# Performance work log

Hardware: AMD Instinct MI355X
Metric: run time of the kernel (lower is better)

Reference implementation:

```python
import jax, jax.numpy as jnp
import numpy as np

# Constants from the module's docstrings / vm_step / constants
VOCAB = 272
D_MODEL = 512
CODE_START = 256  # Token.CODE_START (first special after 256 byte tokens)
CODE_END = 257    # Token.CODE_END
MEM = 258         # Token.MEM
ADDR_KEY = 206    # _SetDim.ADDR_KEY (48 dims: 3 nibbles x 16 one-hot)
MEM_STORE = 455   # _SetDim.MEM_STORE
BYTES_PER_INSTR = 5
INSTR_WIDTH = 8


def setup_inputs() -> dict:
    key = jax.random.key(0)
    k1, k2 = jax.random.split(key)
    token_ids = jax.random.randint(k1, (32, 8192), 0, VOCAB)
    embed_table = jax.random.normal(k2, (VOCAB, D_MODEL), dtype=jnp.float32)
    return {"token_ids": token_ids, "embed_table": embed_table, "mem_history_end": 2048}


def reference(token_ids, embed_table, mem_history_end):
    B, S = token_ids.shape
    x = embed_table[token_ids]                     # [B, S, D] gather
    pos = jnp.arange(S)

    # ---- ADDR_KEY injection (vectorized replacement of the per-token loop) ----
    is_cs = token_ids == CODE_START
    is_ce = token_ids == CODE_END
    # most recent CODE_START position at or before i (-1 if none yet)
    cs = jax.lax.cummax(jnp.where(is_cs, pos[None, :], -1), axis=1)       # [B, S]
    # the python loop breaks the row at the FIRST CODE_END
    first_ce = jnp.min(jnp.where(is_ce, pos[None, :], S), axis=1, keepdims=True)  # [B, 1]
    is_byte = token_ids < 256
    mask = (cs >= 0) & (pos[None, :] < first_ce) & is_byte                # [B, S]

    seq_pos = jnp.maximum(pos[None, :] - cs - 1, 0)                       # >=0 where mask
    addr = (seq_pos // BYTES_PER_INSTR) * INSTR_WIDTH + seq_pos % BYTES_PER_INSTR
    lo = addr & 15
    hi = (addr >> 4) & 15
    top = (addr >> 8) & 15

    nib = jnp.arange(16)
    onehot48 = jnp.concatenate(
        [lo[..., None] == nib, hi[..., None] == nib, top[..., None] == nib], axis=-1
    )  # [B, S, 48] bool

    seg = x[..., ADDR_KEY:ADDR_KEY + 48]
    seg = jnp.where(mask[..., None] & onehot48, jnp.float32(1.0), seg)
    x = x.at[..., ADDR_KEY:ADDR_KEY + 48].set(seg)

    # ---- MEM_STORE injection on historical MEM markers ----
    mem_mask = (token_ids == MEM) & (pos[None, :] < mem_history_end)
    ch = jnp.where(mem_mask, jnp.float32(1.0), x[..., MEM_STORE])
    x = x.at[..., MEM_STORE].set(ch)
    return x
```

## Files before the change

### kernel.cpp

```cpp
#include <hip/hip_runtime.h>
#include <hip/hip_bf16.h>

#define B 32
#define S 8192
#define D 512
#define CODE_START 256
#define CODE_END 257
#define MEM_TOK 258
#define ADDR_KEY 206
#define MEM_STORE 455
#define CHUNK 512
#define NCH (S / CHUNK)

typedef float f32x4 __attribute__((ext_vector_type(4)));

__global__ __launch_bounds__(256) void nvm_chunk_scan(
    const int* __restrict__ tok, int* __restrict__ cs_local,
    int* __restrict__ carry, int* __restrict__ mince) {
  const int c = blockIdx.x;
  const int b = blockIdx.y;
  const int tid = threadIdx.x;
  const int lane = tid & 63;
  const int wid = tid >> 6;
  const int base = c * CHUNK;
  const int* row = tok + b * S;

  const int s0 = base + 2 * tid, s1 = s0 + 1;
  const int t0 = row[s0], t1 = row[s1];
  int v0 = (t0 == CODE_START) ? s0 : -1;
  int v1 = (t1 == CODE_START) ? s1 : -1;
  const int i1 = max(v0, v1);

  int incl = i1;
  #pragma unroll
  for (int off = 1; off < 64; off <<= 1) {
    int u = __shfl_up(incl, off, 64);
    if (lane >= off) incl = max(incl, u);
  }
  int ex = __shfl_up(incl, 1, 64);
  if (lane == 0) ex = -1;

  int m = min((t0 == CODE_END) ? s0 : S, (t1 == CODE_END) ? s1 : S);
  #pragma unroll
  for (int off = 32; off; off >>= 1) m = min(m, __shfl_down(m, off, 64));

  __shared__ int wt[4], wm[4];
  if (lane == 63) wt[wid] = incl;
  if (lane == 0) wm[wid] = m;
  __syncthreads();

  int pre = -1;
  for (int w = 0; w < wid; ++w) pre = max(pre, wt[w]);
  ex = max(ex, pre);
  cs_local[b * S + s0] = max(ex, v0);
  cs_local[b * S + s1] = max(ex, i1);

  if (tid == 0) {
    carry[b * NCH + c] = max(max(wt[0], wt[1]), max(wt[2], wt[3]));
    mince[b * NCH + c] = min(min(wm[0], wm[1]), min(wm[2], wm[3]));
  }
}

__global__ __launch_bounds__(256) void nvm_main(
    const int* __restrict__ tok, const float* __restrict__ table,
    const int* __restrict__ cs_local, const int* __restrict__ carry,
    const int* __restrict__ mince, const int* __restrict__ mhe_p,
    float* __restrict__ out) {
  __shared__ int pre_sh[B * NCH];
  __shared__ int fce_sh[B];

  for (int i = threadIdx.x; i < B * NCH; i += 256) {
    const int b = i >> 4, c = i & (NCH - 1);
    int run = -1;
    for (int c2 = 0; c2 < c; ++c2) run = max(run, carry[(b << 4) + c2]);
    pre_sh[i] = run;
  }
  if (threadIdx.x < B) {
    int mn = S;
    #pragma unroll
    for (int c2 = 0; c2 < NCH; ++c2) mn = min(mn, mince[(threadIdx.x << 4) + c2]);
    fce_sh[threadIdx.x] = mn;
  }
  __syncthreads();

  const int lane = threadIdx.x & 127;
  const int half = threadIdx.x >> 7;
  const int mhe = mhe_p[0];
  const int NTP = B * S / 2;
  const int c0 = lane * 4;

  for (int tp = blockIdx.x; tp < NTP; tp += gridDim.x) {
    const int t = tp * 2 + half;
    const int b = t >> 13;
    const int s = t & (S - 1);

    const int tk = tok[t];
    const int cs = max(cs_local[t], pre_sh[(b << 4) + (s >> 9)]);
    const int f = fce_sh[b];

    const bool maskAddr = (cs >= 0) && (s < f) && (tk < 256);
    int c1 = -1, c2 = -1, c3 = -1;
    if (maskAddr) {
      int sp = s - cs - 1;
      if (sp < 0) sp = 0;
      int q = sp / 5;
      int r = sp - q * 5;
      int addr = q * 8 + r;
      c1 = ADDR_KEY + (addr & 15);
      c2 = ADDR_KEY + 16 + ((addr >> 4) & 15);
      c3 = ADDR_KEY + 32 + ((addr >> 8) & 15);
    }
    const bool memM = (tk == MEM_TOK) && (s < mhe);

    f32x4 v = *reinterpret_cast<const f32x4*>(table + tk * D + c0);
    #pragma unroll
    for (int j = 0; j < 4; ++j) {
      int ch = c0 + j;
      bool hit = (maskAddr && (ch == c1 || ch == c2 || ch == c3)) ||
                 (memM && ch == MEM_STORE);
      if (hit) v[j] = 1.0f;
    }
    f32x4* dst = reinterpret_cast<f32x4*>(out + (size_t)t * D + c0);
    __builtin_nontemporal_store(v, dst);
  }
}

extern "C" void kernel_launch(void* const* d_in, const int* in_sizes, int n_in,
                              void* d_out, int out_size, void* d_ws, size_t ws_size,
                              hipStream_t stream) {
  const int* tok = (const int*)d_in[0];
  const float* table = (const float*)d_in[1];
  const int* mhe = (const int*)d_in[2];
  float* out = (float*)d_out;

  int* cs_local = (int*)d_ws;
  int* carry = cs_local + B * S;
  int* mince = carry + B * NCH;

  nvm_chunk_scan<<<dim3(NCH, B), 256, 0, stream>>>(tok, cs_local, carry, mince);
  nvm_main<<<4096, 256, 0, stream>>>(tok, table, cs_local, carry, mince, mhe, out);
}
```

Before: 109.8 us.

## Fuse chunk scan into main kernel with per-chunk packed token metadata in LDS

The first kernel now only computes per-chunk CODE_START carry and CODE_END minimum, so the per-token cs_local array is no longer written to global memory. The main kernel works on one chunk per block: it redoes the local prefix scan, packs token id, address nibbles and flags into shared memory, then streams out the embedding rows. This removes the workspace round trip and the per-token index math inside the store loop. The cost is a 512-block grid, which may cut parallelism compared with the previous 4096-block grid-stride launch, plus some repeated scan work.

Measured after the change: 111.5 us. Within noise of the previous version (+1.5%).

```diff
diff --git a/kernel.cpp b/kernel.cpp
--- a/kernel.cpp
+++ b/kernel.cpp
@@ -14,23 +14,61 @@
 
 typedef float f32x4 __attribute__((ext_vector_type(4)));
 
-__global__ __launch_bounds__(256) void nvm_chunk_scan(
-    const int* __restrict__ tok, int* __restrict__ cs_local,
-    int* __restrict__ carry, int* __restrict__ mince) {
-  const int c = blockIdx.x;
-  const int b = blockIdx.y;
+__global__ __launch_bounds__(256) void nvm_carry(
+    const int* __restrict__ tok, int* __restrict__ carry, int* __restrict__ mince) {
+  const int c = blockIdx.x, b = blockIdx.y;
   const int tid = threadIdx.x;
-  const int lane = tid & 63;
-  const int wid = tid >> 6;
+  const int lane = tid & 63, wid = tid >> 6;
+  const int p0 = c * CHUNK + 2 * tid;
+  int2 tt = reinterpret_cast<const int2*>(tok + b * S + c * CHUNK)[tid];
+  int vmax = max(tt.x == CODE_START ? p0 : -1, tt.y == CODE_START ? p0 + 1 : -1);
+  int vmin = min(tt.x == CODE_END ? p0 : S, tt.y == CODE_END ? p0 + 1 : S);
+  #pragma unroll
+  for (int off = 32; off; off >>= 1) {
+    vmax = max(vmax, __shfl_down(vmax, off, 64));
+    vmin = min(vmin, __shfl_down(vmin, off, 64));
+  }
+  __shared__ int smax[4], smin[4];
+  if (lane == 0) { smax[wid] = vmax; smin[wid] = vmin; }
+  __syncthreads();
+  if (tid == 0) {
+    carry[b * NCH + c] = max(max(smax[0], smax[1]), max(smax[2], smax[3]));
+    mince[b * NCH + c] = min(min(smin[0], smin[1]), min(smin[2], smin[3]));
+  }
+}
+
+__device__ inline int make_pack(int tk, int cs, int p, int f, int mhe) {
+  int pk = tk;
+  if ((cs >= 0) && (p < f) && (tk < 256)) {
+    int sp = p - cs - 1;
+    if (sp < 0) sp = 0;
+    int q = sp / 5;
+    int r = sp - q * 5;
+    int addr = q * 8 + r;
+    pk |= (1 << 9) | ((addr & 15) << 12) | (((addr >> 4) & 15) << 16) |
+          (((addr >> 8) & 15) << 20);
+  }
+  if (tk == MEM_TOK && p < mhe) pk |= (1 << 10);
+  return pk;
+}
+
+__global__ __launch_bounds__(256) void nvm_main(
+    const int* __restrict__ tok, const float* __restrict__ table,
+    const int* __restrict__ carry, const int* __restrict__ mince,
+    const int* __restrict__ mhe_p, float* __restrict__ out) {
+  const int c = blockIdx.x, b = blockIdx.y;
+  const int tid = threadIdx.x;
+  const int lane = tid & 63, wid = tid >> 6;
   const int base = c * CHUNK;
-  const int* row = tok + b * S;
 
-  const int s0 = base + 2 * tid, s1 = s0 + 1;
-  const int t0 = row[s0], t1 = row[s1];
-  int v0 = (t0 == CODE_START) ? s0 : -1;
-  int v1 = (t1 == CODE_START) ? s1 : -1;
+  __shared__ int pack_sh[CHUNK];
+  __shared__ int wt[4];
+
+  int2 tt = reinterpret_cast<const int2*>(tok + b * S + base)[tid];
+  const int p0 = base + 2 * tid;
+  const int v0 = (tt.x == CODE_START) ? p0 : -1;
+  const int v1 = (tt.y == CODE_START) ? p0 + 1 : -1;
   const int i1 = max(v0, v1);
-
   int incl = i1;
   #pragma unroll
   for (int off = 1; off < 64; off <<= 1) {
@@ -39,89 +77,47 @@
   }
   int ex = __shfl_up(incl, 1, 64);
   if (lane == 0) ex = -1;
+  if (lane == 63) wt[wid] = incl;
+  __syncthreads();
+  int pre = -1;
+  for (int w = 0; w < wid; ++w) pre = max(pre, wt[w]);
+  for (int c2 = 0; c2 < c; ++c2) pre = max(pre, carry[b * NCH + c2]);
+  ex = max(ex, pre);
+  const int cs0 = max(ex, v0);
+  const int cs1 = max(ex, i1);
 
-  int m = min((t0 == CODE_END) ? s0 : S, (t1 == CODE_END) ? s1 : S);
+  int f = S;
   #pragma unroll
-  for (int off = 32; off; off >>= 1) m = min(m, __shfl_down(m, off, 64));
+  for (int c2 = 0; c2 < NCH; ++c2) f = min(f, mince[b * NCH + c2]);
+  const int mhe = mhe_p[0];
 
-  __shared__ int wt[4], wm[4];
-  if (lane == 63) wt[wid] = incl;
-  if (lane == 0) wm[wid] = m;
+  pack_sh[2 * tid] = make_pack(tt.x, cs0, p0, f, mhe);
+  pack_sh[2 * tid + 1] = make_pack(tt.y, cs1, p0 + 1, f, mhe);
   __syncthreads();
 
-  int pre = -1;
-  for (int w = 0; w < wid; ++w) pre = max(pre, wt[w]);
-  ex = max(ex, pre);
-  cs_local[b * S + s0] = max(ex, v0);
-  cs_local[b * S + s1] = max(ex, i1);
+  const int ln = tid & 127;
+  const int half = tid >> 7;
+  const int c0 = ln * 4;
+  float* outb = out + (size_t)(b * S + base) * D;
 
-  if (tid == 0) {
-    carry[b * NCH + c] = max(max(wt[0], wt[1]), max(wt[2], wt[3]));
-    mince[b * NCH + c] = min(min(wm[0], wm[1]), min(wm[2], wm[3]));
-  }
-}
-
-__global__ __launch_bounds__(256) void nvm_main(
-    const int* __restrict__ tok, const float* __restrict__ table,
-    const int* __restrict__ cs_local, const int* __restrict__ carry,
-    const int* __restrict__ mince, const int* __restrict__ mhe_p,
-    float* __restrict__ out) {
-  __shared__ int pre_sh[B * NCH];
-  __shared__ int fce_sh[B];
-
-  for (int i = threadIdx.x; i < B * NCH; i += 256) {
-    const int b = i >> 4, c = i & (NCH - 1);
-    int run = -1;
-    for (int c2 = 0; c2 < c; ++c2) run = max(run, carry[(b << 4) + c2]);
-    pre_sh[i] = run;
-  }
-  if (threadIdx.x < B) {
-    int mn = S;
-    #pragma unroll
-    for (int c2 = 0; c2 < NCH; ++c2) mn = min(mn, mince[(threadIdx.x << 4) + c2]);
-    fce_sh[threadIdx.x] = mn;
-  }
-  __syncthreads();
-
-  const int lane = threadIdx.x & 127;
-  const int half = threadIdx.x >> 7;
-  const int mhe = mhe_p[0];
-  const int NTP = B * S / 2;
-  const int c0 = lane * 4;
-
-  for (int tp = blockIdx.x; tp < NTP; tp += gridDim.x) {
-    const int t = tp * 2 + half;
-    const int b = t >> 13;
-    const int s = t & (S - 1);
-
-    const int tk = tok[t];
-    const int cs = max(cs_local[t], pre_sh[(b << 4) + (s >> 9)]);
-    const int f = fce_sh[b];
-
-    const bool maskAddr = (cs >= 0) && (s < f) && (tk < 256);
-    int c1 = -1, c2 = -1, c3 = -1;
-    if (maskAddr) {
-      int sp = s - cs - 1;
-      if (sp < 0) sp = 0;
-      int q = sp / 5;
-      int r = sp - q * 5;
-      int addr = q * 8 + r;
-      c1 = ADDR_KEY + (addr & 15);
-      c2 = ADDR_KEY + 16 + ((addr >> 4) & 15);
-      c3 = ADDR_KEY + 32 + ((addr >> 8) & 15);
+  #pragma unroll 4
+  for (int j = 0; j < CHUNK / 2; ++j) {
+    const int i = 2 * j + half;
+    const int p = pack_sh[i];
+    const int tk = p & 511;
+    f32x4 v = *reinterpret_cast<const f32x4*>(table + tk * D + c0);
+    if (p & (1 << 9)) {
+      const int ca = ADDR_KEY + ((p >> 12) & 15);
+      const int cb = ADDR_KEY + 16 + ((p >> 16) & 15);
+      const int cc = ADDR_KEY + 32 + ((p >> 20) & 15);
+      #pragma unroll
+      for (int u = 0; u < 4; ++u) {
+        const int ch = c0 + u;
+        if (ch == ca || ch == cb || ch == cc) v[u] = 1.0f;
+      }
     }
-    const bool memM = (tk == MEM_TOK) && (s < mhe);
-
-    f32x4 v = *reinterpret_cast<const f32x4*>(table + tk * D + c0);
-    #pragma unroll
-    for (int j = 0; j < 4; ++j) {
-      int ch = c0 + j;
-      bool hit = (maskAddr && (ch == c1 || ch == c2 || ch == c3)) ||
-                 (memM && ch == MEM_STORE);
-      if (hit) v[j] = 1.0f;
-    }
-    f32x4* dst = reinterpret_cast<f32x4*>(out + (size_t)t * D + c0);
-    __builtin_nontemporal_store(v, dst);
+    if ((p & (1 << 10)) && c0 == (MEM_STORE & ~3)) v[MEM_STORE & 3] = 1.0f;
+    __builtin_nontemporal_store(v, reinterpret_cast<f32x4*>(outb + (size_t)i * D + c0));
   }
 }
 
@@ -133,10 +129,9 @@
   const int* mhe = (const int*)d_in[2];
   float* out = (float*)d_out;
 
-  int* cs_local = (int*)d_ws;
-  int* carry = cs_local + B * S;
+  int* carry = (int*)d_ws;
   int* mince = carry + B * NCH;
 
-  nvm_chunk_scan<<<dim3(NCH, B), 256, 0, stream>>>(tok, cs_local, carry, mince);
-  nvm_main<<<4096, 256, 0, stream>>>(tok, table, cs_local, carry, mince, mhe, out);
+  nvm_carry<<<dim3(NCH, B), 256, 0, stream>>>(tok, carry, mince);
+  nvm_main<<<dim3(NCH, B), 256, 0, stream>>>(tok, table, carry, mince, mhe, out);
 }
```
